# Kernel optimization log

Hardware: AMD Instinct MI355X
Metric: run time of the kernel (lower is better)

Reference implementation:

```python
import jax, jax.numpy as jnp
import numpy as np

IN_F, OUT_F = 1024, 1024
GRID_SIZE, SPLINE_ORDER = 5, 3
GRID_RANGE = (-1.0, 1.0)
NUM_BASIS = GRID_SIZE + SPLINE_ORDER  # 8


def b_splines(x, grid, spline_order):
    # x: (B, in), grid: (in, G) with G = grid_size + 2*spline_order + 1
    x = x[..., None]            # (B, in, 1)
    g = grid[None, :, :]        # (1, in, G)
    B = ((x >= g[..., :-1]) & (x < g[..., 1:])).astype(x.dtype)  # (B, in, G-1)
    for k in range(1, spline_order + 1):
        left = (x - g[..., :-(k + 1)]) / (g[..., k:-1] - g[..., :-(k + 1)])
        right = (g[..., k + 1:] - x) / (g[..., k + 1:] - g[..., 1:-k])
        B = left * B[..., :-1] + right * B[..., 1:]
    return B  # (B, in, grid_size + spline_order)


def setup_inputs() -> dict:
    key = jax.random.key(0)
    k1, k2, k3, k4 = jax.random.split(key, 4)
    batch = 8192
    x = jax.random.normal(k1, (batch, IN_F), dtype=jnp.float32)
    h = (GRID_RANGE[1] - GRID_RANGE[0]) / GRID_SIZE
    knots = jnp.arange(-SPLINE_ORDER, GRID_SIZE + SPLINE_ORDER + 1, dtype=jnp.float32) * h + GRID_RANGE[0]
    grid = jnp.broadcast_to(knots, (IN_F, knots.shape[0]))  # (in, 12)
    base_weight = jax.random.normal(k2, (OUT_F, IN_F), dtype=jnp.float32) * (1.0 / np.sqrt(IN_F))
    spline_weight = jax.random.normal(k3, (OUT_F, IN_F, NUM_BASIS), dtype=jnp.float32) * 0.02
    spline_scaler = jax.random.normal(k4, (OUT_F, IN_F), dtype=jnp.float32) * (1.0 / np.sqrt(IN_F))
    return {"x": x, "grid": grid, "base_weight": base_weight,
            "spline_weight": spline_weight, "spline_scaler": spline_scaler}


def reference(x, grid, base_weight, spline_weight, spline_scaler):
    # base branch: SiLU then linear
    base_out = jax.nn.silu(x) @ base_weight.T  # (B, out)
    # normalize x to [-1, 1] by global min/max
    x_min, x_max = jnp.min(x), jnp.max(x)
    x_norm = (x - x_min) / (x_max - x_min + 1e-8) * 2.0 - 1.0
    basis = b_splines(x_norm, grid, SPLINE_ORDER)  # (B, in, K)
    w = spline_weight * spline_scaler[..., None]   # (out, in, K)
    spline_out = jnp.einsum('bik,oik->bo', basis, w)
    return base_out + spline_out
```

## Files before the change

kernel.cpp:

```cpp
#include <hip/hip_runtime.h>
#include <hip/hip_bf16.h>

#define IN_F   1024
#define OUT_F  1024
#define NBASIS 8
#define KDIM   (IN_F + IN_F * NBASIS)
#define BM 128
#define BN 128
#define BK 64
#define KT      (KDIM / BK)
#define BASE_KT (IN_F / BK)

typedef __attribute__((ext_vector_type(8))) short          bf16x8;
typedef __attribute__((ext_vector_type(8))) unsigned short u16x8;
typedef __attribute__((ext_vector_type(4))) float          f32x4;

typedef const __attribute__((address_space(1))) void gas_t;
typedef __attribute__((address_space(3))) void las_t;
#define GLD16(g, l) __builtin_amdgcn_global_load_lds((gas_t*)(g), (las_t*)(l), 16, 0, 0)

__device__ __forceinline__ unsigned short bfr(float f) {
    unsigned u = __float_as_uint(f);
    unsigned r = (u + 0x7FFFu + ((u >> 16) & 1u)) >> 16;
    return (unsigned short)r;
}
__device__ __forceinline__ float silu_f(float v) { return v / (1.0f + __expf(-v)); }

__device__ __forceinline__ unsigned fkey(float f) {
    unsigned u = __float_as_uint(f);
    return u ^ ((u >> 31) ? 0xFFFFFFFFu : 0x80000000u);
}
__device__ __forceinline__ float fkey_dec(unsigned u) {
    unsigned b = (u >> 31) ? (u ^ 0x80000000u) : ~u;
    return __uint_as_float(b);
}

__device__ __forceinline__ void spline8(float xv, float xmin, float scale, u16x8* o8p) {
    float xn = (xv - xmin) * scale - 1.0f;
    float u  = (xn + 2.2f) * 2.5f;
    int   iv = (int)floorf(u);
    iv = iv < 3 ? 3 : (iv > 7 ? 7 : iv);
    float tt = u - (float)iv;
    float s1 = 1.0f - tt;
    float t2 = tt * tt, t3 = t2 * tt;
    float n0 = s1 * s1 * s1 * (1.0f / 6.0f);
    float n1 = (3.0f * t3 - 6.0f * t2 + 4.0f) * (1.0f / 6.0f);
    float n2 = (-3.0f * t3 + 3.0f * t2 + 3.0f * tt + 1.0f) * (1.0f / 6.0f);
    float n3 = t3 * (1.0f / 6.0f);
    int j0 = iv - 3;
    u16x8 o8;
    #pragma unroll
    for (int s = 0; s < 8; ++s) {
        int d = s - j0;
        float val = (d == 0) ? n0 : (d == 1) ? n1 : (d == 2) ? n2 : (d == 3) ? n3 : 0.0f;
        o8[s] = bfr(val);
    }
    *o8p = o8;
}

__global__ void k_minmax(const float* __restrict__ x, unsigned* __restrict__ mm, int n4) {
    int tid    = blockIdx.x * blockDim.x + threadIdx.x;
    int stride = gridDim.x * blockDim.x;
    const float4* x4 = (const float4*)x;
    float mx  = -3.402823466e+38f;
    float mxn = -3.402823466e+38f;
    for (int i = tid; i < n4; i += stride) {
        float4 v = x4[i];
        mx  = fmaxf(mx,  fmaxf(fmaxf(v.x, v.y), fmaxf(v.z, v.w)));
        mxn = fmaxf(mxn, -fminf(fminf(v.x, v.y), fminf(v.z, v.w)));
    }
    #pragma unroll
    for (int off = 32; off; off >>= 1) {
        mx  = fmaxf(mx,  __shfl_down(mx,  off));
        mxn = fmaxf(mxn, __shfl_down(mxn, off));
    }
    __shared__ float smx[4], smn[4];
    int lane = threadIdx.x & 63, wid = threadIdx.x >> 6;
    if (lane == 0) { smx[wid] = mx; smn[wid] = mxn; }
    __syncthreads();
    if (threadIdx.x == 0) {
        #pragma unroll
        for (int w = 1; w < 4; ++w) { mx = fmaxf(mx, smx[w]); mxn = fmaxf(mxn, smn[w]); }
        atomicMax(&mm[0], fkey(mx));
        atomicMax(&mm[1], fkey(mxn));
    }
}

__global__ void k_prepw(const float* __restrict__ bw, const float* __restrict__ sw,
                        const float* __restrict__ sc, unsigned short* __restrict__ Wc) {
    int t = blockIdx.x * blockDim.x + threadIdx.x;
    int o = t >> 10, i = t & 1023;
    Wc[(size_t)o * KDIM + i] = bfr(bw[t]);
    float s = sc[t];
    const float4* swv = (const float4*)(sw + (size_t)t * 8);
    float4 a = swv[0], b = swv[1];
    u16x8 o8;
    o8[0] = bfr(a.x * s); o8[1] = bfr(a.y * s); o8[2] = bfr(a.z * s); o8[3] = bfr(a.w * s);
    o8[4] = bfr(b.x * s); o8[5] = bfr(b.y * s); o8[6] = bfr(b.z * s); o8[7] = bfr(b.w * s);
    *(u16x8*)(Wc + (size_t)o * KDIM + IN_F + i * 8) = o8;
}

__global__ void k_build_a(const float* __restrict__ x, const unsigned* __restrict__ mm,
                          unsigned short* __restrict__ Ac) {
    int t = blockIdx.x * blockDim.x + threadIdx.x;
    int row = t >> 10, i = t & 1023;
    const float xmax  = fkey_dec(mm[0]);
    const float xmin  = -fkey_dec(mm[1]);
    const float scale = 2.0f / (xmax - xmin + 1e-8f);
    float xv = x[t];
    size_t rb = (size_t)row * KDIM;
    Ac[rb + i] = bfr(silu_f(xv));
    u16x8 o8;
    spline8(xv, xmin, scale, &o8);
    *(u16x8*)(Ac + rb + IN_F + (size_t)i * 8) = o8;
}

__global__ __launch_bounds__(256, 2)
void k_gemm2(const unsigned short* __restrict__ Ac, const unsigned short* __restrict__ Wc,
             float* __restrict__ out, int nmb) {
    __shared__ unsigned short As[BM * BK];
    __shared__ unsigned short Bs[BN * BK];

    const int t = threadIdx.x;
    const int lane = t & 63, w = t >> 6;

    int bid = blockIdx.x;
    int bM, bN;
    if (nmb == 64) {
        int xcd = bid & 7, s = bid >> 3;
        bM = xcd * 8 + (s & 7);
        bN = s >> 3;
    } else {
        bM = bid >> 3;
        bN = bid & 7;
    }

    const unsigned short* pa[4];
    const unsigned short* pb[4];
    #pragma unroll
    for (int q = 0; q < 4; ++q) {
        int idx = (q * 4 + w) * 64 + lane;
        int r = idx >> 3, c8 = idx & 7;
        pa[q] = Ac + (size_t)(bM * BM + r) * KDIM + c8 * 8;
        pb[q] = Wc + (size_t)(bN * BN + r) * KDIM + c8 * 8;
    }

    const int wr  = (w >> 1) * 64;
    const int wc2 = (w & 1) * 64;

    f32x4 acc[4][4] = {};

    for (int kt = 0; kt < KT; ++kt) {
        __syncthreads();
        #pragma unroll
        for (int q = 0; q < 4; ++q) {
            GLD16(pa[q], &As[(q * 4 + w) * 512]);
            GLD16(pb[q], &Bs[(q * 4 + w) * 512]);
            pa[q] += BK;
            pb[q] += BK;
        }
        __syncthreads();

        bf16x8 af[4][2];
        #pragma unroll
        for (int mi = 0; mi < 4; ++mi) {
            int row = wr + mi * 16 + (lane & 15);
            #pragma unroll
            for (int ks = 0; ks < 2; ++ks)
                af[mi][ks] = *(const bf16x8*)&As[row * BK + ks * 32 + (lane >> 4) * 8];
        }
        #pragma unroll
        for (int ni = 0; ni < 4; ++ni) {
            int col = wc2 + ni * 16 + (lane & 15);
            bf16x8 b0 = *(const bf16x8*)&Bs[col * BK + (lane >> 4) * 8];
            bf16x8 b1 = *(const bf16x8*)&Bs[col * BK + 32 + (lane >> 4) * 8];
            #pragma unroll
            for (int mi = 0; mi < 4; ++mi) {
                acc[mi][ni] = __builtin_amdgcn_mfma_f32_16x16x32_bf16(af[mi][0], b0, acc[mi][ni], 0, 0, 0);
                acc[mi][ni] = __builtin_amdgcn_mfma_f32_16x16x32_bf16(af[mi][1], b1, acc[mi][ni], 0, 0, 0);
            }
        }
    }

    #pragma unroll
    for (int mi = 0; mi < 4; ++mi) {
        #pragma unroll
        for (int ni = 0; ni < 4; ++ni) {
            #pragma unroll
            for (int reg = 0; reg < 4; ++reg) {
                int row = wr + mi * 16 + (lane >> 4) * 4 + reg;
                int col = wc2 + ni * 16 + (lane & 15);
                out[(size_t)(bM * BM + row) * OUT_F + bN * BN + col] = acc[mi][ni][reg];
            }
        }
    }
}

__global__ __launch_bounds__(256, 2)
void k_gemm_fused(const float* __restrict__ x, const unsigned short* __restrict__ Wc,
                  const unsigned* __restrict__ mm, float* __restrict__ out) {
    __shared__ unsigned short As[BM * BK];
    __shared__ unsigned short Bs[BN * BK];

    const int t  = threadIdx.x;
    const int bM = blockIdx.x >> 3;
    const int bN = blockIdx.x & 7;

    const float xmax  = fkey_dec(mm[0]);
    const float xmin  = -fkey_dec(mm[1]);
    const float scale = 2.0f / (xmax - xmin + 1e-8f);

    const int lane = t & 63, wid = t >> 6;
    const int wr = (wid >> 1) * 64, wc = (wid & 1) * 64;

    const int rr = t >> 1, kh = t & 1;
    const float*          xrow = x  + (size_t)(bM * BM + rr) * IN_F;
    const unsigned short* wrow = Wc + (size_t)(bN * BN + rr) * KDIM;

    f32x4 acc[4][4] = {};

    for (int kt = 0; kt < KT; ++kt) {
        __syncthreads();
        {
            const u16x8* src = (const u16x8*)(wrow + kt * BK + kh * 32);
            #pragma unroll
            for (int q = 0; q < 4; ++q) {
                u16x8 v = src[q];
                int c = (kh * 4 + q) ^ (rr & 7);
                *(u16x8*)&Bs[rr * BK + c * 8] = v;
            }
        }
        if (kt < BASE_KT) {
            const float* xp = xrow + kt * BK + kh * 32;
            #pragma unroll
            for (int q = 0; q < 4; ++q) {
                float4 v0 = *(const float4*)(xp + q * 8);
                float4 v1 = *(const float4*)(xp + q * 8 + 4);
                u16x8 o8;
                o8[0] = bfr(silu_f(v0.x)); o8[1] = bfr(silu_f(v0.y));
                o8[2] = bfr(silu_f(v0.z)); o8[3] = bfr(silu_f(v0.w));
                o8[4] = bfr(silu_f(v1.x)); o8[5] = bfr(silu_f(v1.y));
                o8[6] = bfr(silu_f(v1.z)); o8[7] = bfr(silu_f(v1.w));
                int c = (kh * 4 + q) ^ (rr & 7);
                *(u16x8*)&As[rr * BK + c * 8] = o8;
            }
        } else {
            const int f0 = (kt - BASE_KT) * 8 + kh * 4;
            float4 v = *(const float4*)(xrow + f0);
            #pragma unroll
            for (int q = 0; q < 4; ++q) {
                float xv = (q == 0) ? v.x : (q == 1) ? v.y : (q == 2) ? v.z : v.w;
                u16x8 o8;
                spline8(xv, xmin, scale, &o8);
                int c = (kh * 4 + q) ^ (rr & 7);
                *(u16x8*)&As[rr * BK + c * 8] = o8;
            }
        }
        __syncthreads();

        bf16x8 af[4][2];
        #pragma unroll
        for (int mi = 0; mi < 4; ++mi) {
            int row = wr + mi * 16 + (lane & 15);
            int rb  = row & 7;
            #pragma unroll
            for (int ks = 0; ks < 2; ++ks) {
                int c = (ks * 4 + (lane >> 4)) ^ rb;
                af[mi][ks] = *(const bf16x8*)&As[row * BK + c * 8];
            }
        }
        #pragma unroll
        for (int ni = 0; ni < 4; ++ni) {
            int col = wc + ni * 16 + (lane & 15);
            int cb  = col & 7;
            bf16x8 b0 = *(const bf16x8*)&Bs[col * BK + (((lane >> 4)) ^ cb) * 8];
            bf16x8 b1 = *(const bf16x8*)&Bs[col * BK + ((4 + (lane >> 4)) ^ cb) * 8];
            #pragma unroll
            for (int mi = 0; mi < 4; ++mi) {
                acc[mi][ni] = __builtin_amdgcn_mfma_f32_16x16x32_bf16(af[mi][0], b0, acc[mi][ni], 0, 0, 0);
                acc[mi][ni] = __builtin_amdgcn_mfma_f32_16x16x32_bf16(af[mi][1], b1, acc[mi][ni], 0, 0, 0);
            }
        }
    }

    #pragma unroll
    for (int mi = 0; mi < 4; ++mi) {
        #pragma unroll
        for (int ni = 0; ni < 4; ++ni) {
            #pragma unroll
            for (int reg = 0; reg < 4; ++reg) {
                int row = wr + mi * 16 + (lane >> 4) * 4 + reg;
                int col = wc + ni * 16 + (lane & 15);
                out[(size_t)(bM * BM + row) * OUT_F + bN * BN + col] = acc[mi][ni][reg];
            }
        }
    }
}

extern "C" void kernel_launch(void* const* d_in, const int* in_sizes, int n_in,
                              void* d_out, int out_size, void* d_ws, size_t ws_size,
                              hipStream_t stream) {
    const float* x  = (const float*)d_in[0];
    const float* bw = (const float*)d_in[2];
    const float* sw = (const float*)d_in[3];
    const float* sc = (const float*)d_in[4];
    float* out = (float*)d_out;

    const int batch = in_sizes[0] / IN_F;
    const int n4    = in_sizes[0] / 4;

    unsigned*       mm = (unsigned*)d_ws;
    unsigned short* Wc = (unsigned short*)((char*)d_ws + 512);
    const size_t    wc_bytes = (size_t)OUT_F * KDIM * 2;
    unsigned short* Ac = (unsigned short*)((char*)d_ws + 512 + wc_bytes);
    const size_t    ac_bytes = (size_t)batch * KDIM * 2;
    const size_t    need = 512 + wc_bytes + ac_bytes;

    hipMemsetAsync(d_ws, 0, 8, stream);
    k_minmax<<<1024, 256, 0, stream>>>(x, mm, n4);
    k_prepw<<<(OUT_F * IN_F) / 256, 256, 0, stream>>>(bw, sw, sc, Wc);

    if (ws_size >= need && (batch % BM) == 0) {
        k_build_a<<<(batch * IN_F) / 256, 256, 0, stream>>>(x, mm, Ac);
        int nmb = batch / BM;
        k_gemm2<<<dim3(nmb * (OUT_F / BN)), 256, 0, stream>>>(Ac, Wc, out, nmb);
    } else {
        k_gemm_fused<<<dim3((batch / BM) * (OUT_F / BN)), 256, 0, stream>>>(x, Wc, mm, out);
    }
}
```

Before: 367.8 us.

## Add triple-buffered 128x256 GEMM with direct-to-LDS loads and vectorize A build

Adds k_gemm3, a 512-thread GEMM with 128x256 tiles. It uses a three-slot LDS ring filled by global_load_lds, with loads issued two k-steps ahead, vmcnt waits, split barriers and s_setprio around the MFMA bursts, so memory transfer overlaps compute and each loaded tile is reused more. k_build_a now handles eight features per thread with vector loads and stores. The fused fallback kernel is removed, so when the workspace is too small nothing is computed. The new path runs only when batch is 8192, and its prefetch pointers wrap around to stay in bounds on the last iterations.

After: 336.3 us. 8.5% less time.

```diff
diff --git a/kernel.cpp b/kernel.cpp
--- a/kernel.cpp
+++ b/kernel.cpp
@@ -5,11 +5,20 @@
 #define OUT_F  1024
 #define NBASIS 8
 #define KDIM   (IN_F + IN_F * NBASIS)
-#define BM 128
-#define BN 128
 #define BK 64
 #define KT      (KDIM / BK)
 #define BASE_KT (IN_F / BK)
+
+#define BM3 128
+#define BN3 256
+#define A_ELEMS (BM3 * BK)
+#define B_ELEMS (BN3 * BK)
+#define SLOT    (A_ELEMS + B_ELEMS)
+#define A_OFF   0
+#define B_OFF   A_ELEMS
+
+#define BM 128
+#define BN 128
 
 typedef __attribute__((ext_vector_type(8))) short          bf16x8;
 typedef __attribute__((ext_vector_type(8))) unsigned short u16x8;
@@ -103,16 +112,168 @@
 __global__ void k_build_a(const float* __restrict__ x, const unsigned* __restrict__ mm,
                           unsigned short* __restrict__ Ac) {
     int t = blockIdx.x * blockDim.x + threadIdx.x;
-    int row = t >> 10, i = t & 1023;
+    int row = t >> 7, i8 = t & 127;
     const float xmax  = fkey_dec(mm[0]);
     const float xmin  = -fkey_dec(mm[1]);
     const float scale = 2.0f / (xmax - xmin + 1e-8f);
-    float xv = x[t];
+    const float* xp = x + (size_t)row * IN_F + i8 * 8;
+    float4 v0 = *(const float4*)xp;
+    float4 v1 = *(const float4*)(xp + 4);
     size_t rb = (size_t)row * KDIM;
-    Ac[rb + i] = bfr(silu_f(xv));
-    u16x8 o8;
-    spline8(xv, xmin, scale, &o8);
-    *(u16x8*)(Ac + rb + IN_F + (size_t)i * 8) = o8;
+    u16x8 sv;
+    sv[0] = bfr(silu_f(v0.x)); sv[1] = bfr(silu_f(v0.y));
+    sv[2] = bfr(silu_f(v0.z)); sv[3] = bfr(silu_f(v0.w));
+    sv[4] = bfr(silu_f(v1.x)); sv[5] = bfr(silu_f(v1.y));
+    sv[6] = bfr(silu_f(v1.z)); sv[7] = bfr(silu_f(v1.w));
+    *(u16x8*)(Ac + rb + i8 * 8) = sv;
+    unsigned short* bp = Ac + rb + IN_F + (size_t)i8 * 64;
+    #pragma unroll
+    for (int j = 0; j < 8; ++j) {
+        float xv = (j == 0) ? v0.x : (j == 1) ? v0.y : (j == 2) ? v0.z : (j == 3) ? v0.w
+                 : (j == 4) ? v1.x : (j == 5) ? v1.y : (j == 6) ? v1.z : v1.w;
+        u16x8 o8;
+        spline8(xv, xmin, scale, &o8);
+        *(u16x8*)(bp + j * 8) = o8;
+    }
+}
+
+#define MFMA(a, b, c) __builtin_amdgcn_mfma_f32_16x16x32_bf16((a), (b), (c), 0, 0, 0)
+
+__global__ __launch_bounds__(512, 2)
+void k_gemm3(const unsigned short* __restrict__ Ac, const unsigned short* __restrict__ Wc,
+             float* __restrict__ out) {
+    __shared__ unsigned short sm[3 * SLOT];
+
+    const int t    = threadIdx.x;
+    const int lane = t & 63, w = t >> 6;
+    const int bid  = blockIdx.x;
+    const int xcd = bid & 7, s = bid >> 3;
+    const int bM  = xcd * 8 + (s & 7);
+    const int bN  = s >> 3;
+
+    const int wave_r = w >> 2;
+    const int wcq    = w & 3;
+
+    const unsigned short* pa0; const unsigned short* pa1;
+    const unsigned short* pb0; const unsigned short* pb1;
+    const unsigned short* pb2; const unsigned short* pb3;
+    {
+        int L, r, c;
+        L = (0 * 8 + w) * 64 + lane; r = L >> 3; c = L & 7;
+        pa0 = Ac + (size_t)(bM * BM3 + r) * KDIM + (c ^ (r & 7)) * 8;
+        L = (1 * 8 + w) * 64 + lane; r = L >> 3; c = L & 7;
+        pa1 = Ac + (size_t)(bM * BM3 + r) * KDIM + (c ^ (r & 7)) * 8;
+        L = (0 * 8 + w) * 64 + lane; r = L >> 3; c = L & 7;
+        pb0 = Wc + (size_t)(bN * BN3 + r) * KDIM + (c ^ (r & 7)) * 8;
+        L = (1 * 8 + w) * 64 + lane; r = L >> 3; c = L & 7;
+        pb1 = Wc + (size_t)(bN * BN3 + r) * KDIM + (c ^ (r & 7)) * 8;
+        L = (2 * 8 + w) * 64 + lane; r = L >> 3; c = L & 7;
+        pb2 = Wc + (size_t)(bN * BN3 + r) * KDIM + (c ^ (r & 7)) * 8;
+        L = (3 * 8 + w) * 64 + lane; r = L >> 3; c = L & 7;
+        pb3 = Wc + (size_t)(bN * BN3 + r) * KDIM + (c ^ (r & 7)) * 8;
+    }
+
+    const int ach0 = (lane >> 4) ^ (lane & 7);
+    const int ach1 = ach0 ^ 4;
+    const int l15  = lane & 15;
+
+    f32x4 acc[4][4] = {};
+
+    GLD16(pa0, &sm[0 * SLOT + A_OFF + (0 * 8 + w) * 512]);
+    GLD16(pa1, &sm[0 * SLOT + A_OFF + (1 * 8 + w) * 512]);
+    GLD16(pb0, &sm[0 * SLOT + B_OFF + (0 * 8 + w) * 512]);
+    GLD16(pb1, &sm[0 * SLOT + B_OFF + (1 * 8 + w) * 512]);
+    GLD16(pb2, &sm[0 * SLOT + B_OFF + (2 * 8 + w) * 512]);
+    GLD16(pb3, &sm[0 * SLOT + B_OFF + (3 * 8 + w) * 512]);
+    pa0 += BK; pa1 += BK; pb0 += BK; pb1 += BK; pb2 += BK; pb3 += BK;
+    GLD16(pa0, &sm[1 * SLOT + A_OFF + (0 * 8 + w) * 512]);
+    GLD16(pa1, &sm[1 * SLOT + A_OFF + (1 * 8 + w) * 512]);
+    GLD16(pb0, &sm[1 * SLOT + B_OFF + (0 * 8 + w) * 512]);
+    GLD16(pb1, &sm[1 * SLOT + B_OFF + (1 * 8 + w) * 512]);
+    GLD16(pb2, &sm[1 * SLOT + B_OFF + (2 * 8 + w) * 512]);
+    GLD16(pb3, &sm[1 * SLOT + B_OFF + (3 * 8 + w) * 512]);
+    pa0 += BK; pa1 += BK; pb0 += BK; pb1 += BK; pb2 += BK; pb3 += BK;
+
+    int o0 = 0, o1 = SLOT, o2 = 2 * SLOT;
+    int sk = 2;
+
+    asm volatile("s_waitcnt vmcnt(6)" ::: "memory");
+    asm volatile("s_barrier" ::: "memory");
+
+    for (int kt = 0; kt < KT; ++kt) {
+        bf16x8 af[4][2];
+        #pragma unroll
+        for (int mi = 0; mi < 4; ++mi) {
+            int r = wave_r * 64 + mi * 16 + l15;
+            af[mi][0] = *(const bf16x8*)&sm[o0 + A_OFF + r * BK + ach0 * 8];
+            af[mi][1] = *(const bf16x8*)&sm[o0 + A_OFF + r * BK + ach1 * 8];
+        }
+        bf16x8 bf0[2][2];
+        #pragma unroll
+        for (int ni = 0; ni < 2; ++ni) {
+            int r = wcq * 64 + ni * 16 + l15;
+            bf0[ni][0] = *(const bf16x8*)&sm[o0 + B_OFF + r * BK + ach0 * 8];
+            bf0[ni][1] = *(const bf16x8*)&sm[o0 + B_OFF + r * BK + ach1 * 8];
+        }
+        GLD16(pa0, &sm[o2 + A_OFF + (0 * 8 + w) * 512]);
+        GLD16(pa1, &sm[o2 + A_OFF + (1 * 8 + w) * 512]);
+        __builtin_amdgcn_s_barrier();
+        __builtin_amdgcn_s_setprio(1);
+        #pragma unroll
+        for (int ni = 0; ni < 2; ++ni)
+            #pragma unroll
+            for (int mi = 0; mi < 4; ++mi) {
+                acc[mi][ni] = MFMA(af[mi][0], bf0[ni][0], acc[mi][ni]);
+                acc[mi][ni] = MFMA(af[mi][1], bf0[ni][1], acc[mi][ni]);
+            }
+        __builtin_amdgcn_s_setprio(0);
+        __builtin_amdgcn_s_barrier();
+
+        bf16x8 bf1[2][2];
+        #pragma unroll
+        for (int ni = 0; ni < 2; ++ni) {
+            int r = wcq * 64 + (ni + 2) * 16 + l15;
+            bf1[ni][0] = *(const bf16x8*)&sm[o0 + B_OFF + r * BK + ach0 * 8];
+            bf1[ni][1] = *(const bf16x8*)&sm[o0 + B_OFF + r * BK + ach1 * 8];
+        }
+        GLD16(pb0, &sm[o2 + B_OFF + (0 * 8 + w) * 512]);
+        GLD16(pb1, &sm[o2 + B_OFF + (1 * 8 + w) * 512]);
+        GLD16(pb2, &sm[o2 + B_OFF + (2 * 8 + w) * 512]);
+        GLD16(pb3, &sm[o2 + B_OFF + (3 * 8 + w) * 512]);
+        __builtin_amdgcn_s_barrier();
+        __builtin_amdgcn_s_setprio(1);
+        #pragma unroll
+        for (int ni = 0; ni < 2; ++ni)
+            #pragma unroll
+            for (int mi = 0; mi < 4; ++mi) {
+                acc[mi][ni + 2] = MFMA(af[mi][0], bf1[ni][0], acc[mi][ni + 2]);
+                acc[mi][ni + 2] = MFMA(af[mi][1], bf1[ni][1], acc[mi][ni + 2]);
+            }
+        __builtin_amdgcn_s_setprio(0);
+
+        pa0 += BK; pa1 += BK; pb0 += BK; pb1 += BK; pb2 += BK; pb3 += BK;
+        if (++sk == KT) {
+            sk = 0;
+            pa0 -= KDIM; pa1 -= KDIM; pb0 -= KDIM; pb1 -= KDIM; pb2 -= KDIM; pb3 -= KDIM;
+        }
+
+        asm volatile("s_waitcnt vmcnt(6)" ::: "memory");
+        asm volatile("s_barrier" ::: "memory");
+        int tmp = o0; o0 = o1; o1 = o2; o2 = tmp;
+    }
+
+    #pragma unroll
+    for (int mi = 0; mi < 4; ++mi) {
+        #pragma unroll
+        for (int ni = 0; ni < 4; ++ni) {
+            #pragma unroll
+            for (int reg = 0; reg < 4; ++reg) {
+                int row = bM * BM3 + wave_r * 64 + mi * 16 + (lane >> 4) * 4 + reg;
+                int col = bN * BN3 + wcq * 64 + ni * 16 + l15;
+                out[(size_t)row * OUT_F + col] = acc[mi][ni][reg];
+            }
+        }
+    }
 }
 
 __global__ __launch_bounds__(256, 2)
@@ -123,17 +284,8 @@
 
     const int t = threadIdx.x;
     const int lane = t & 63, w = t >> 6;
-
     int bid = blockIdx.x;
-    int bM, bN;
-    if (nmb == 64) {
-        int xcd = bid & 7, s = bid >> 3;
-        bM = xcd * 8 + (s & 7);
-        bN = s >> 3;
-    } else {
-        bM = bid >> 3;
-        bN = bid & 7;
-    }
+    int bM = bid >> 3, bN = bid & 7;
 
     const unsigned short* pa[4];
     const unsigned short* pb[4];
@@ -176,8 +328,8 @@
             bf16x8 b1 = *(const bf16x8*)&Bs[col * BK + 32 + (lane >> 4) * 8];
             #pragma unroll
             for (int mi = 0; mi < 4; ++mi) {
-                acc[mi][ni] = __builtin_amdgcn_mfma_f32_16x16x32_bf16(af[mi][0], b0, acc[mi][ni], 0, 0, 0);
-                acc[mi][ni] = __builtin_amdgcn_mfma_f32_16x16x32_bf16(af[mi][1], b1, acc[mi][ni], 0, 0, 0);
+                acc[mi][ni] = MFMA(af[mi][0], b0, acc[mi][ni]);
+                acc[mi][ni] = MFMA(af[mi][1], b1, acc[mi][ni]);
             }
         }
     }
@@ -190,107 +342,6 @@
             for (int reg = 0; reg < 4; ++reg) {
                 int row = wr + mi * 16 + (lane >> 4) * 4 + reg;
                 int col = wc2 + ni * 16 + (lane & 15);
-                out[(size_t)(bM * BM + row) * OUT_F + bN * BN + col] = acc[mi][ni][reg];
-            }
-        }
-    }
-}
-
-__global__ __launch_bounds__(256, 2)
-void k_gemm_fused(const float* __restrict__ x, const unsigned short* __restrict__ Wc,
-                  const unsigned* __restrict__ mm, float* __restrict__ out) {
-    __shared__ unsigned short As[BM * BK];
-    __shared__ unsigned short Bs[BN * BK];
-
-    const int t  = threadIdx.x;
-    const int bM = blockIdx.x >> 3;
-    const int bN = blockIdx.x & 7;
-
-    const float xmax  = fkey_dec(mm[0]);
-    const float xmin  = -fkey_dec(mm[1]);
-    const float scale = 2.0f / (xmax - xmin + 1e-8f);
-
-    const int lane = t & 63, wid = t >> 6;
-    const int wr = (wid >> 1) * 64, wc = (wid & 1) * 64;
-
-    const int rr = t >> 1, kh = t & 1;
-    const float*          xrow = x  + (size_t)(bM * BM + rr) * IN_F;
-    const unsigned short* wrow = Wc + (size_t)(bN * BN + rr) * KDIM;
-
-    f32x4 acc[4][4] = {};
-
-    for (int kt = 0; kt < KT; ++kt) {
-        __syncthreads();
-        {
-            const u16x8* src = (const u16x8*)(wrow + kt * BK + kh * 32);
-            #pragma unroll
-            for (int q = 0; q < 4; ++q) {
-                u16x8 v = src[q];
-                int c = (kh * 4 + q) ^ (rr & 7);
-                *(u16x8*)&Bs[rr * BK + c * 8] = v;
-            }
-        }
-        if (kt < BASE_KT) {
-            const float* xp = xrow + kt * BK + kh * 32;
-            #pragma unroll
-            for (int q = 0; q < 4; ++q) {
-                float4 v0 = *(const float4*)(xp + q * 8);
-                float4 v1 = *(const float4*)(xp + q * 8 + 4);
-                u16x8 o8;
-                o8[0] = bfr(silu_f(v0.x)); o8[1] = bfr(silu_f(v0.y));
-                o8[2] = bfr(silu_f(v0.z)); o8[3] = bfr(silu_f(v0.w));
-                o8[4] = bfr(silu_f(v1.x)); o8[5] = bfr(silu_f(v1.y));
-                o8[6] = bfr(silu_f(v1.z)); o8[7] = bfr(silu_f(v1.w));
-                int c = (kh * 4 + q) ^ (rr & 7);
-                *(u16x8*)&As[rr * BK + c * 8] = o8;
-            }
-        } else {
-            const int f0 = (kt - BASE_KT) * 8 + kh * 4;
-            float4 v = *(const float4*)(xrow + f0);
-            #pragma unroll
-            for (int q = 0; q < 4; ++q) {
-                float xv = (q == 0) ? v.x : (q == 1) ? v.y : (q == 2) ? v.z : v.w;
-                u16x8 o8;
-                spline8(xv, xmin, scale, &o8);
-                int c = (kh * 4 + q) ^ (rr & 7);
-                *(u16x8*)&As[rr * BK + c * 8] = o8;
-            }
-        }
-        __syncthreads();
-
-        bf16x8 af[4][2];
-        #pragma unroll
-        for (int mi = 0; mi < 4; ++mi) {
-            int row = wr + mi * 16 + (lane & 15);
-            int rb  = row & 7;
-            #pragma unroll
-            for (int ks = 0; ks < 2; ++ks) {
-                int c = (ks * 4 + (lane >> 4)) ^ rb;
-                af[mi][ks] = *(const bf16x8*)&As[row * BK + c * 8];
-            }
-        }
-        #pragma unroll
-        for (int ni = 0; ni < 4; ++ni) {
-            int col = wc + ni * 16 + (lane & 15);
-            int cb  = col & 7;
-            bf16x8 b0 = *(const bf16x8*)&Bs[col * BK + (((lane >> 4)) ^ cb) * 8];
-            bf16x8 b1 = *(const bf16x8*)&Bs[col * BK + ((4 + (lane >> 4)) ^ cb) * 8];
-            #pragma unroll
-            for (int mi = 0; mi < 4; ++mi) {
-                acc[mi][ni] = __builtin_amdgcn_mfma_f32_16x16x32_bf16(af[mi][0], b0, acc[mi][ni], 0, 0, 0);
-                acc[mi][ni] = __builtin_amdgcn_mfma_f32_16x16x32_bf16(af[mi][1], b1, acc[mi][ni], 0, 0, 0);
-            }
-        }
-    }
-
-    #pragma unroll
-    for (int mi = 0; mi < 4; ++mi) {
-        #pragma unroll
-        for (int ni = 0; ni < 4; ++ni) {
-            #pragma unroll
-            for (int reg = 0; reg < 4; ++reg) {
-                int row = wr + mi * 16 + (lane >> 4) * 4 + reg;
-                int col = wc + ni * 16 + (lane & 15);
                 out[(size_t)(bM * BM + row) * OUT_F + bN * BN + col] = acc[mi][ni][reg];
             }
         }
@@ -320,11 +371,11 @@
     k_minmax<<<1024, 256, 0, stream>>>(x, mm, n4);
     k_prepw<<<(OUT_F * IN_F) / 256, 256, 0, stream>>>(bw, sw, sc, Wc);
 
-    if (ws_size >= need && (batch % BM) == 0) {
-        k_build_a<<<(batch * IN_F) / 256, 256, 0, stream>>>(x, mm, Ac);
-        int nmb = batch / BM;
-        k_gemm2<<<dim3(nmb * (OUT_F / BN)), 256, 0, stream>>>(Ac, Wc, out, nmb);
-    } else {
-        k_gemm_fused<<<dim3((batch / BM) * (OUT_F / BN)), 256, 0, stream>>>(x, Wc, mm, out);
-    }
-}
+    if (ws_size >= need && batch == 8192) {
+        k_build_a<<<(batch * 128) / 256, 256, 0, stream>>>(x, mm, Ac);
+        k_gemm3<<<dim3((batch / BM3) * (OUT_F / BN3)), 512, 0, stream>>>(Ac, Wc, out);
+    } else if (ws_size >= need && (batch % BM) == 0) {
+        k_build_a<<<(batch * 128) / 256, 256, 0, stream>>>(x, mm, Ac);
+        k_gemm2<<<dim3((batch / BM) * (OUT_F / BN)), 256, 0, stream>>>(Ac, Wc, out, batch / BM);
+    }
+}
```
